# Kernel optimization log

Hardware: AMD Instinct MI355X
Metric: run time of the kernel (lower is better)

## Reference

```python
import jax, jax.numpy as jnp
import numpy as np

B, S, H, E = 4, 4096, 4096, 64
EPS = 1e-6


def setup_inputs() -> dict:
    key = jax.random.key(0)
    k1, k2 = jax.random.split(key)
    hidden_states = jax.random.normal(k1, (B, S, H), dtype=jnp.float32)
    gate_w = jax.random.normal(k2, (E, H), dtype=jnp.float32) * 0.02
    return {"hidden_states": hidden_states, "gate_w": gate_w, "C": 512}


def reference(hidden_states, gate_w, C):
    b, s, h = hidden_states.shape
    e = gate_w.shape[0]
    flat = hidden_states.reshape(-1, h)                    # [BS, H]
    logits = jnp.einsum('th,eh->te', flat, gate_w)          # [BS, E]
    # deterministic=True -> no noise added
    probs = jax.nn.softmax(logits, axis=-1)                 # [BS, E]
    # expert-choice: each expert picks top-C tokens
    _, topC_idx = jax.lax.top_k(logits.T, C)                # [E, C] token indices
    routing_map = jnp.zeros_like(logits).at[
        topC_idx, jnp.arange(e)[:, None]].set(1.0)          # [BS, E]
    # normalize_weights=True
    probs = probs * routing_map
    probs = probs / (probs.sum(axis=-1, keepdims=True) + EPS)
    # aux losses (torch .std() is unbiased -> ddof=1)
    importance = probs.sum(axis=0)                          # [E]
    imp_loss = (jnp.std(importance, ddof=1) / (importance.mean() + EPS)) ** 2
    load = routing_map.sum(axis=0)                          # [E]
    load_loss = (jnp.std(load, ddof=1) / (load.mean() + EPS)) ** 2
    aux_loss = imp_loss + load_loss
    return (probs.reshape(b, s, e), routing_map.reshape(b, s, e), aux_loss)
```

## Files before the change

### kernel.cpp

```cpp
#include <hip/hip_runtime.h>
#include <hip/hip_bf16.h>

#define BS 16384
#define HDIM 4096
#define NE 64
#define KC 64
#define TT 64
#define CAP 512
#define DELTA 2e-3f

typedef __bf16 bf16x8 __attribute__((ext_vector_type(8)));
typedef float f32x4 __attribute__((ext_vector_type(4)));
union Frag { uint4 q; bf16x8 v; };

__device__ inline unsigned f2key(float f) {
    unsigned u = __float_as_uint(f);
    return (u & 0x80000000u) ? ~u : (u | 0x80000000u);
}
__device__ inline float key2f(unsigned k) {
    unsigned u = (k & 0x80000000u) ? (k ^ 0x80000000u) : ~k;
    return __uint_as_float(u);
}
__device__ inline unsigned pack_hi(float a, float b) {
    return (__float_as_uint(a) >> 16) | (__float_as_uint(b) & 0xFFFF0000u);
}
__device__ inline float bf16_resid(float a) {
    return a - __uint_as_float(__float_as_uint(a) & 0xFFFF0000u);
}

__global__ __launch_bounds__(256) void k0_init(const float* __restrict__ W,
                                               unsigned short* __restrict__ Wh,
                                               unsigned short* __restrict__ Wl,
                                               unsigned* __restrict__ win_g,
                                               double* __restrict__ imp_g) {
    const int gtid = blockIdx.x * 256 + threadIdx.x;
    const size_t f = (size_t)gtid * 4;
    float4 w = *(const float4*)(W + f);
    uint2 hh, ll;
    hh.x = pack_hi(w.x, w.y); hh.y = pack_hi(w.z, w.w);
    ll.x = pack_hi(bf16_resid(w.x), bf16_resid(w.y));
    ll.y = pack_hi(bf16_resid(w.z), bf16_resid(w.w));
    *(uint2*)(Wh + f) = hh;
    *(uint2*)(Wl + f) = ll;
    if (gtid < NE * CAP) win_g[gtid] = 0u;
    if (gtid < NE) imp_g[gtid] = 0.0;
}

__global__ __launch_bounds__(512, 1) void k1_gemm(const float* __restrict__ A,
                                                  const unsigned short* __restrict__ Wh,
                                                  const unsigned short* __restrict__ Wl,
                                                  float* __restrict__ Lg,
                                                  unsigned* __restrict__ KeyT) {
    __shared__ __align__(16) unsigned short sbuf[2 * 18432];

    const int tid = threadIdx.x;
    const int T0 = blockIdx.x * TT;

    const int arow = tid >> 3, aseg = tid & 7;
    const int wr = (tid >> 3) & 63, wblk = tid & 7;

    const int lane = tid & 63, w = tid >> 6;
    const int m = lane & 15, q = lane >> 4;
    const int wm = w & 3;
    const int wn = w >> 2;

    const float* Aprow = A + (size_t)(T0 + arow) * HDIM + aseg * 8;
    const unsigned short* Whrow = Wh + (size_t)wr * HDIM + wblk * 8;
    const unsigned short* Wlrow = Wl + (size_t)wr * HDIM + wblk * 8;

    f32x4 acc[2] = {{0.f, 0.f, 0.f, 0.f}, {0.f, 0.f, 0.f, 0.f}};

    float4 pa0 = *(const float4*)(Aprow);
    float4 pa1 = *(const float4*)(Aprow + 4);
    uint4 pw0 = *(const uint4*)(Whrow);
    uint4 pw1 = *(const uint4*)(Wlrow);

    {
        unsigned short* B = sbuf;
        uint4 H, L;
        H.x = pack_hi(pa0.x, pa0.y); H.y = pack_hi(pa0.z, pa0.w);
        H.z = pack_hi(pa1.x, pa1.y); H.w = pack_hi(pa1.z, pa1.w);
        L.x = pack_hi(bf16_resid(pa0.x), bf16_resid(pa0.y));
        L.y = pack_hi(bf16_resid(pa0.z), bf16_resid(pa0.w));
        L.z = pack_hi(bf16_resid(pa1.x), bf16_resid(pa1.y));
        L.w = pack_hi(bf16_resid(pa1.z), bf16_resid(pa1.w));
        *(uint4*)(B + arow * 72 + aseg * 8) = H;
        *(uint4*)(B + 4608 + arow * 72 + aseg * 8) = L;
        *(uint4*)(B + 9216 + wr * 72 + wblk * 8) = pw0;
        *(uint4*)(B + 13824 + wr * 72 + wblk * 8) = pw1;
    }

    for (int c = 0; c < HDIM / KC; ++c) {
        if (c + 1 < HDIM / KC) {
            const int c0 = (c + 1) * KC;
            pa0 = *(const float4*)(Aprow + c0);
            pa1 = *(const float4*)(Aprow + c0 + 4);
            pw0 = *(const uint4*)(Whrow + c0);
            pw1 = *(const uint4*)(Wlrow + c0);
        }
        __syncthreads();
        {
            const unsigned short* B = sbuf + (c & 1) * 18432;
            const unsigned short* Ash = B + (wm * 16 + m) * 72;
            const unsigned short* Asl = Ash + 4608;
#pragma unroll
            for (int kh = 0; kh < 2; ++kh) {
                const int ko = kh * 32 + q * 8;
                Frag ah, al;
                ah.q = *(const uint4*)(Ash + ko);
                al.q = *(const uint4*)(Asl + ko);
#pragma unroll
                for (int nt = 0; nt < 2; ++nt) {
                    const int er = wn * 32 + nt * 16 + m;
                    Frag bh, bl;
                    bh.q = *(const uint4*)(B + 9216 + er * 72 + ko);
                    bl.q = *(const uint4*)(B + 13824 + er * 72 + ko);
                    acc[nt] = __builtin_amdgcn_mfma_f32_16x16x32_bf16(ah.v, bh.v, acc[nt], 0, 0, 0);
                    acc[nt] = __builtin_amdgcn_mfma_f32_16x16x32_bf16(al.v, bh.v, acc[nt], 0, 0, 0);
                    acc[nt] = __builtin_amdgcn_mfma_f32_16x16x32_bf16(ah.v, bl.v, acc[nt], 0, 0, 0);
                }
            }
        }
        if (c + 1 < HDIM / KC) {
            unsigned short* B = sbuf + ((c + 1) & 1) * 18432;
            uint4 H, L;
            H.x = pack_hi(pa0.x, pa0.y); H.y = pack_hi(pa0.z, pa0.w);
            H.z = pack_hi(pa1.x, pa1.y); H.w = pack_hi(pa1.z, pa1.w);
            L.x = pack_hi(bf16_resid(pa0.x), bf16_resid(pa0.y));
            L.y = pack_hi(bf16_resid(pa0.z), bf16_resid(pa0.w));
            L.z = pack_hi(bf16_resid(pa1.x), bf16_resid(pa1.y));
            L.w = pack_hi(bf16_resid(pa1.z), bf16_resid(pa1.w));
            *(uint4*)(B + arow * 72 + aseg * 8) = H;
            *(uint4*)(B + 4608 + arow * 72 + aseg * 8) = L;
            *(uint4*)(B + 9216 + wr * 72 + wblk * 8) = pw0;
            *(uint4*)(B + 13824 + wr * 72 + wblk * 8) = pw1;
        }
    }

    __syncthreads();
    float* Sc = (float*)sbuf;
#pragma unroll
    for (int nt = 0; nt < 2; ++nt) {
        const int e = wn * 32 + nt * 16 + m;
#pragma unroll
        for (int r = 0; r < 4; ++r) {
            const int tl = wm * 16 + q * 4 + r;
            const float v = acc[nt][r];
            Sc[tl * 68 + e] = v;
            Lg[(size_t)(T0 + tl) * NE + e] = v;
        }
    }
    __syncthreads();
    {
        const int e = tid >> 3, jj = tid & 7;
        unsigned kk[8];
#pragma unroll
        for (int r = 0; r < 8; ++r) kk[r] = f2key(Sc[(jj * 8 + r) * 68 + e]);
        uint4 v0 = {kk[0], kk[1], kk[2], kk[3]}, v1 = {kk[4], kk[5], kk[6], kk[7]};
        unsigned* dst = KeyT + (size_t)e * BS + T0 + jj * 8;
        *(uint4*)dst = v0;
        *(uint4*)(dst + 4) = v1;
    }
}

__global__ __launch_bounds__(1024) void k2_select(const unsigned* __restrict__ KeyT,
                                                  const int* __restrict__ Cptr,
                                                  unsigned* __restrict__ khi_g,
                                                  int* __restrict__ needed_g,
                                                  int* __restrict__ ncand_g,
                                                  int* __restrict__ cand_g) {
    const int e = blockIdx.x, tid = threadIdx.x;
    const int wid = tid >> 6, lane = tid & 63;
    const int C = *Cptr;
    const unsigned* col = KeyT + (size_t)e * BS;

    unsigned key[16];
#pragma unroll
    for (int j = 0; j < 16; ++j) key[j] = col[j * 1024 + tid];

    __shared__ int sred[16];
    __shared__ int s_tot;
    __shared__ int s_nc;

    unsigned K = 0;
    for (int b = 31; b >= 0; --b) {
        const unsigned T = K | (1u << b);
        int c = 0;
#pragma unroll
        for (int j = 0; j < 16; ++j) c += (key[j] >= T);
#pragma unroll
        for (int off = 32; off; off >>= 1) c += __shfl_xor(c, off);
        if (lane == 0) sred[wid] = c;
        __syncthreads();
        if (wid == 0) {
            int v = (lane < 16) ? sred[lane] : 0;
            v += __shfl_xor(v, 1); v += __shfl_xor(v, 2);
            v += __shfl_xor(v, 4); v += __shfl_xor(v, 8);
            if (lane == 0) s_tot = v;
        }
        __syncthreads();
        if (s_tot >= C) K = T;
        __syncthreads();
    }

    const float vT = key2f(K);
    const unsigned khi = f2key(vT + DELTA);
    const unsigned klo = f2key(vT - DELTA);

    int nd = 0;
#pragma unroll
    for (int j = 0; j < 16; ++j) nd += (key[j] > khi);
#pragma unroll
    for (int off = 32; off; off >>= 1) nd += __shfl_xor(nd, off);
    if (lane == 0) sred[wid] = nd;
    if (tid == 0) s_nc = 0;
    __syncthreads();
    if (wid == 0) {
        int v = (lane < 16) ? sred[lane] : 0;
        v += __shfl_xor(v, 1); v += __shfl_xor(v, 2);
        v += __shfl_xor(v, 4); v += __shfl_xor(v, 8);
        if (lane == 0) s_tot = v;
    }
    __syncthreads();
#pragma unroll
    for (int j = 0; j < 16; ++j) {
        if (key[j] >= klo && key[j] <= khi) {
            const int pos = atomicAdd(&s_nc, 1);
            if (pos < CAP) cand_g[(size_t)e * CAP + pos] = j * 1024 + tid;
        }
    }
    __syncthreads();
    if (tid == 0) {
        khi_g[e] = khi;
        needed_g[e] = C - s_tot;
        ncand_g[e] = (s_nc < CAP) ? s_nc : CAP;
    }
}

__global__ __launch_bounds__(256) void k2b_resolve(const float* __restrict__ A,
                                                   const float* __restrict__ W,
                                                   const int* __restrict__ needed_g,
                                                   const int* __restrict__ ncand_g,
                                                   const int* __restrict__ cand_g,
                                                   unsigned* __restrict__ win_g) {
    const int e = blockIdx.x, tid = threadIdx.x, w = tid >> 6, lane = tid & 63;
    int n = ncand_g[e]; if (n > CAP) n = CAP;
    int need = needed_g[e]; if (need > n) need = n; if (need < 0) need = 0;
    __shared__ double sval[CAP];
    __shared__ int sidx[CAP];
    const float* Wr = W + (size_t)e * HDIM;
    for (int c = w; c < n; c += 4) {
        const int t = cand_g[(size_t)e * CAP + c];
        const float* Ar = A + (size_t)t * HDIM;
        double ps = 0.0;
#pragma unroll 8
        for (int j = 0; j < HDIM / 64; ++j)
            ps += (double)Ar[j * 64 + lane] * (double)Wr[j * 64 + lane];
#pragma unroll
        for (int off = 32; off; off >>= 1) ps += __shfl_xor(ps, off);
        if (lane == 0) { sval[c] = ps; sidx[c] = t; }
    }
    __syncthreads();
    if (tid == 0) {
        for (int s = 0; s < need; ++s) {
            int best = -1;
            for (int c = 0; c < n; ++c) {
                if (sidx[c] < 0) continue;
                if (best < 0 || sval[c] > sval[best] ||
                    (sval[c] == sval[best] && sidx[c] < sidx[best]))
                    best = c;
            }
            const int t = sidx[best];
            win_g[(size_t)e * CAP + (t >> 5)] |= (1u << (t & 31));
            sidx[best] = -1;
        }
    }
}

__global__ __launch_bounds__(256) void k3_softmax(const float* __restrict__ Lg,
                                                  const unsigned* __restrict__ khi_g,
                                                  const unsigned* __restrict__ win_g,
                                                  float* __restrict__ probs,
                                                  float* __restrict__ out_map,
                                                  double* __restrict__ imp_g) {
    const int tid = threadIdx.x, w = tid >> 6, e = tid & 63, b = blockIdx.x;
    __shared__ unsigned skhi[64];
    __shared__ double sim[4][64];
    if (tid < 64) skhi[tid] = khi_g[tid];
    __syncthreads();
    const unsigned kh = skhi[e];
    double accim = 0.0;
#pragma unroll
    for (int it = 0; it < 4; ++it) {
        const int t = b * 16 + w * 4 + it;
        const float x = Lg[(size_t)t * NE + e];
        const unsigned key = f2key(x);
        float mfl;
        if (key > kh) mfl = 1.f;
        else mfl = (float)((win_g[(size_t)e * CAP + (t >> 5)] >> (t & 31)) & 1u);
        const float ev = expf(x);
        const float evm = ev * mfl;
        float s1 = ev, s2 = evm;
#pragma unroll
        for (int off = 32; off; off >>= 1) {
            s1 += __shfl_xor(s1, off);
            s2 += __shfl_xor(s2, off);
        }
        const float o = evm / (s2 + 1e-6f * s1);
        probs[(size_t)t * NE + e] = o;
        out_map[(size_t)t * NE + e] = mfl;
        accim += (double)o;
    }
    sim[w][e] = accim;
    __syncthreads();
    if (w == 0) atomicAdd(&imp_g[e], sim[0][e] + sim[1][e] + sim[2][e] + sim[3][e]);
}

__global__ __launch_bounds__(64) void k4_aux(const double* __restrict__ imp_g,
                                             float* __restrict__ out_aux) {
    const int e = threadIdx.x;
    const double v = imp_g[e];
    double s = v;
#pragma unroll
    for (int off = 32; off; off >>= 1) s += __shfl_xor(s, off);
    const double mean = s / 64.0;
    const double d = v - mean;
    double ss = d * d;
#pragma unroll
    for (int off = 32; off; off >>= 1) ss += __shfl_xor(ss, off);
    if (e == 0) {
        const double var = ss / 63.0;
        const double dn = mean + 1e-6;
        out_aux[0] = (float)(var / (dn * dn));
    }
}

extern "C" void kernel_launch(void* const* d_in, const int* in_sizes, int n_in,
                              void* d_out, int out_size, void* d_ws, size_t ws_size,
                              hipStream_t stream) {
    const float* A = (const float*)d_in[0];
    const float* W = (const float*)d_in[1];
    const int* Cptr = (const int*)d_in[2];

    float* out_probs = (float*)d_out;
    float* out_map = out_probs + (size_t)BS * NE;
    float* out_aux = out_map + (size_t)BS * NE;

    char* wsb = (char*)d_ws;
    float*          Lg     = (float*)wsb;
    unsigned*       KeyT   = (unsigned*)(wsb + (4ull << 20));
    unsigned short* Wh     = (unsigned short*)(wsb + (8ull << 20));
    unsigned short* Wl     = (unsigned short*)(wsb + (8ull << 20) + (512ull << 10));
    int*            cand   = (int*)(wsb + (9ull << 20));
    unsigned*       win    = (unsigned*)(wsb + (9ull << 20) + (128ull << 10));
    unsigned*       khi_g  = (unsigned*)(wsb + (9ull << 20) + (256ull << 10));
    int*            needed = (int*)(wsb + (9ull << 20) + (257ull << 10));
    int*            ncand  = (int*)(wsb + (9ull << 20) + (258ull << 10));
    double*         imp_g  = (double*)(wsb + (9ull << 20) + (259ull << 10));

    k0_init<<<256, 256, 0, stream>>>(W, Wh, Wl, win, imp_g);
    k1_gemm<<<BS / TT, 512, 0, stream>>>(A, Wh, Wl, Lg, KeyT);
    k2_select<<<NE, 1024, 0, stream>>>(KeyT, Cptr, khi_g, needed, ncand, cand);
    k2b_resolve<<<NE, 256, 0, stream>>>(A, W, needed, ncand, cand, win);
    k3_softmax<<<BS / 16, 256, 0, stream>>>(Lg, khi_g, win, out_probs, out_map, imp_g);
    k4_aux<<<1, 64, 0, stream>>>(imp_g, out_aux);
}
```

Baseline: 473.9 us.

## Shrink GEMM token tile, use per-token win bitmask, drop importance atomics

```diff
diff --git a/kernel.cpp b/kernel.cpp
--- a/kernel.cpp
+++ b/kernel.cpp
@@ -5,7 +5,7 @@
 #define HDIM 4096
 #define NE 64
 #define KC 64
-#define TT 64
+#define TT 32
 #define CAP 512
 #define DELTA 2e-3f
 
@@ -31,8 +31,7 @@
 __global__ __launch_bounds__(256) void k0_init(const float* __restrict__ W,
                                                unsigned short* __restrict__ Wh,
                                                unsigned short* __restrict__ Wl,
-                                               unsigned* __restrict__ win_g,
-                                               double* __restrict__ imp_g) {
+                                               unsigned long long* __restrict__ win_t) {
     const int gtid = blockIdx.x * 256 + threadIdx.x;
     const size_t f = (size_t)gtid * 4;
     float4 w = *(const float4*)(W + f);
@@ -42,38 +41,40 @@
     ll.y = pack_hi(bf16_resid(w.z), bf16_resid(w.w));
     *(uint2*)(Wh + f) = hh;
     *(uint2*)(Wl + f) = ll;
-    if (gtid < NE * CAP) win_g[gtid] = 0u;
-    if (gtid < NE) imp_g[gtid] = 0.0;
-}
-
-__global__ __launch_bounds__(512, 1) void k1_gemm(const float* __restrict__ A,
+    if (gtid < BS) win_t[gtid] = 0ull;
+}
+
+__global__ __launch_bounds__(256, 2) void k1_gemm(const float* __restrict__ A,
                                                   const unsigned short* __restrict__ Wh,
                                                   const unsigned short* __restrict__ Wl,
                                                   float* __restrict__ Lg,
                                                   unsigned* __restrict__ KeyT) {
-    __shared__ __align__(16) unsigned short sbuf[2 * 18432];
+    __shared__ __align__(16) unsigned short sbuf[2 * 13824];
 
     const int tid = threadIdx.x;
     const int T0 = blockIdx.x * TT;
 
     const int arow = tid >> 3, aseg = tid & 7;
-    const int wr = (tid >> 3) & 63, wblk = tid & 7;
 
     const int lane = tid & 63, w = tid >> 6;
     const int m = lane & 15, q = lane >> 4;
-    const int wm = w & 3;
-    const int wn = w >> 2;
+    const int wm = w & 1;
+    const int wn = w >> 1;
 
     const float* Aprow = A + (size_t)(T0 + arow) * HDIM + aseg * 8;
-    const unsigned short* Whrow = Wh + (size_t)wr * HDIM + wblk * 8;
-    const unsigned short* Wlrow = Wl + (size_t)wr * HDIM + wblk * 8;
 
     f32x4 acc[2] = {{0.f, 0.f, 0.f, 0.f}, {0.f, 0.f, 0.f, 0.f}};
 
     float4 pa0 = *(const float4*)(Aprow);
     float4 pa1 = *(const float4*)(Aprow + 4);
-    uint4 pw0 = *(const uint4*)(Whrow);
-    uint4 pw1 = *(const uint4*)(Wlrow);
+    uint4 pwh[2], pwl[2];
+#pragma unroll
+    for (int i = 0; i < 2; ++i) {
+        const int u = i * 256 + tid;
+        const int r = u >> 3, blk = u & 7;
+        pwh[i] = *(const uint4*)(Wh + (size_t)r * HDIM + blk * 8);
+        pwl[i] = *(const uint4*)(Wl + (size_t)r * HDIM + blk * 8);
+    }
 
     {
         unsigned short* B = sbuf;
@@ -85,9 +86,14 @@
         L.z = pack_hi(bf16_resid(pa1.x), bf16_resid(pa1.y));
         L.w = pack_hi(bf16_resid(pa1.z), bf16_resid(pa1.w));
         *(uint4*)(B + arow * 72 + aseg * 8) = H;
-        *(uint4*)(B + 4608 + arow * 72 + aseg * 8) = L;
-        *(uint4*)(B + 9216 + wr * 72 + wblk * 8) = pw0;
-        *(uint4*)(B + 13824 + wr * 72 + wblk * 8) = pw1;
+        *(uint4*)(B + 2304 + arow * 72 + aseg * 8) = L;
+#pragma unroll
+        for (int i = 0; i < 2; ++i) {
+            const int u = i * 256 + tid;
+            const int r = u >> 3, blk = u & 7;
+            *(uint4*)(B + 4608 + r * 72 + blk * 8) = pwh[i];
+            *(uint4*)(B + 9216 + r * 72 + blk * 8) = pwl[i];
+        }
     }
 
     for (int c = 0; c < HDIM / KC; ++c) {
@@ -95,14 +101,19 @@
             const int c0 = (c + 1) * KC;
             pa0 = *(const float4*)(Aprow + c0);
             pa1 = *(const float4*)(Aprow + c0 + 4);
-            pw0 = *(const uint4*)(Whrow + c0);
-            pw1 = *(const uint4*)(Wlrow + c0);
+#pragma unroll
+            for (int i = 0; i < 2; ++i) {
+                const int u = i * 256 + tid;
+                const int r = u >> 3, blk = u & 7;
+                pwh[i] = *(const uint4*)(Wh + (size_t)r * HDIM + c0 + blk * 8);
+                pwl[i] = *(const uint4*)(Wl + (size_t)r * HDIM + c0 + blk * 8);
+            }
         }
         __syncthreads();
         {
-            const unsigned short* B = sbuf + (c & 1) * 18432;
+            const unsigned short* B = sbuf + (c & 1) * 13824;
             const unsigned short* Ash = B + (wm * 16 + m) * 72;
-            const unsigned short* Asl = Ash + 4608;
+            const unsigned short* Asl = Ash + 2304;
 #pragma unroll
             for (int kh = 0; kh < 2; ++kh) {
                 const int ko = kh * 32 + q * 8;
@@ -113,8 +124,8 @@
                 for (int nt = 0; nt < 2; ++nt) {
                     const int er = wn * 32 + nt * 16 + m;
                     Frag bh, bl;
-                    bh.q = *(const uint4*)(B + 9216 + er * 72 + ko);
-                    bl.q = *(const uint4*)(B + 13824 + er * 72 + ko);
+                    bh.q = *(const uint4*)(B + 4608 + er * 72 + ko);
+                    bl.q = *(const uint4*)(B + 9216 + er * 72 + ko);
                     acc[nt] = __builtin_amdgcn_mfma_f32_16x16x32_bf16(ah.v, bh.v, acc[nt], 0, 0, 0);
                     acc[nt] = __builtin_amdgcn_mfma_f32_16x16x32_bf16(al.v, bh.v, acc[nt], 0, 0, 0);
                     acc[nt] = __builtin_amdgcn_mfma_f32_16x16x32_bf16(ah.v, bl.v, acc[nt], 0, 0, 0);
@@ -122,7 +133,7 @@
             }
         }
         if (c + 1 < HDIM / KC) {
-            unsigned short* B = sbuf + ((c + 1) & 1) * 18432;
+            unsigned short* B = sbuf + ((c + 1) & 1) * 13824;
             uint4 H, L;
             H.x = pack_hi(pa0.x, pa0.y); H.y = pack_hi(pa0.z, pa0.w);
             H.z = pack_hi(pa1.x, pa1.y); H.w = pack_hi(pa1.z, pa1.w);
@@ -131,9 +142,14 @@
             L.z = pack_hi(bf16_resid(pa1.x), bf16_resid(pa1.y));
             L.w = pack_hi(bf16_resid(pa1.z), bf16_resid(pa1.w));
             *(uint4*)(B + arow * 72 + aseg * 8) = H;
-            *(uint4*)(B + 4608 + arow * 72 + aseg * 8) = L;
-            *(uint4*)(B + 9216 + wr * 72 + wblk * 8) = pw0;
-            *(uint4*)(B + 13824 + wr * 72 + wblk * 8) = pw1;
+            *(uint4*)(B + 2304 + arow * 72 + aseg * 8) = L;
+#pragma unroll
+            for (int i = 0; i < 2; ++i) {
+                const int u = i * 256 + tid;
+                const int r = u >> 3, blk = u & 7;
+                *(uint4*)(B + 4608 + r * 72 + blk * 8) = pwh[i];
+                *(uint4*)(B + 9216 + r * 72 + blk * 8) = pwl[i];
+            }
         }
     }
 
@@ -152,7 +168,7 @@
     }
     __syncthreads();
     {
-        const int e = tid >> 3, jj = tid & 7;
+        const int e = tid >> 2, jj = tid & 3;
         unsigned kk[8];
 #pragma unroll
         for (int r = 0; r < 8; ++r) kk[r] = f2key(Sc[(jj * 8 + r) * 68 + e]);
@@ -242,7 +258,7 @@
                                                    const int* __restrict__ needed_g,
                                                    const int* __restrict__ ncand_g,
                                                    const int* __restrict__ cand_g,
-                                                   unsigned* __restrict__ win_g) {
+                                                   unsigned long long* __restrict__ win_t) {
     const int e = blockIdx.x, tid = threadIdx.x, w = tid >> 6, lane = tid & 63;
     int n = ncand_g[e]; if (n > CAP) n = CAP;
     int need = needed_g[e]; if (need > n) need = n; if (need < 0) need = 0;
@@ -271,7 +287,7 @@
                     best = c;
             }
             const int t = sidx[best];
-            win_g[(size_t)e * CAP + (t >> 5)] |= (1u << (t & 31));
+            atomicOr(&win_t[t], 1ull << e);
             sidx[best] = -1;
         }
     }
@@ -279,10 +295,10 @@
 
 __global__ __launch_bounds__(256) void k3_softmax(const float* __restrict__ Lg,
                                                   const unsigned* __restrict__ khi_g,
-                                                  const unsigned* __restrict__ win_g,
+                                                  const unsigned long long* __restrict__ win_t,
                                                   float* __restrict__ probs,
                                                   float* __restrict__ out_map,
-                                                  double* __restrict__ imp_g) {
+                                                  double* __restrict__ imp_partial) {
     const int tid = threadIdx.x, w = tid >> 6, e = tid & 63, b = blockIdx.x;
     __shared__ unsigned skhi[64];
     __shared__ double sim[4][64];
@@ -291,13 +307,13 @@
     const unsigned kh = skhi[e];
     double accim = 0.0;
 #pragma unroll
-    for (int it = 0; it < 4; ++it) {
-        const int t = b * 16 + w * 4 + it;
+    for (int it = 0; it < 16; ++it) {
+        const int t = b * 64 + it * 4 + w;
         const float x = Lg[(size_t)t * NE + e];
         const unsigned key = f2key(x);
         float mfl;
         if (key > kh) mfl = 1.f;
-        else mfl = (float)((win_g[(size_t)e * CAP + (t >> 5)] >> (t & 31)) & 1u);
+        else mfl = (float)((win_t[t] >> e) & 1ull);
         const float ev = expf(x);
         const float evm = ev * mfl;
         float s1 = ev, s2 = evm;
@@ -313,13 +329,15 @@
     }
     sim[w][e] = accim;
     __syncthreads();
-    if (w == 0) atomicAdd(&imp_g[e], sim[0][e] + sim[1][e] + sim[2][e] + sim[3][e]);
-}
-
-__global__ __launch_bounds__(64) void k4_aux(const double* __restrict__ imp_g,
+    if (w == 0)
+        imp_partial[(size_t)b * NE + e] = sim[0][e] + sim[1][e] + sim[2][e] + sim[3][e];
+}
+
+__global__ __launch_bounds__(64) void k4_aux(const double* __restrict__ imp_partial,
                                              float* __restrict__ out_aux) {
     const int e = threadIdx.x;
-    const double v = imp_g[e];
+    double v = 0.0;
+    for (int b = 0; b < 256; ++b) v += imp_partial[(size_t)b * NE + e];
     double s = v;
 #pragma unroll
     for (int off = 32; off; off >>= 1) s += __shfl_xor(s, off);
@@ -347,21 +365,21 @@
     float* out_aux = out_map + (size_t)BS * NE;
 
     char* wsb = (char*)d_ws;
-    float*          Lg     = (float*)wsb;
-    unsigned*       KeyT   = (unsigned*)(wsb + (4ull << 20));
-    unsigned short* Wh     = (unsigned short*)(wsb + (8ull << 20));
-    unsigned short* Wl     = (unsigned short*)(wsb + (8ull << 20) + (512ull << 10));
-    int*            cand   = (int*)(wsb + (9ull << 20));
-    unsigned*       win    = (unsigned*)(wsb + (9ull << 20) + (128ull << 10));
-    unsigned*       khi_g  = (unsigned*)(wsb + (9ull << 20) + (256ull << 10));
-    int*            needed = (int*)(wsb + (9ull << 20) + (257ull << 10));
-    int*            ncand  = (int*)(wsb + (9ull << 20) + (258ull << 10));
-    double*         imp_g  = (double*)(wsb + (9ull << 20) + (259ull << 10));
-
-    k0_init<<<256, 256, 0, stream>>>(W, Wh, Wl, win, imp_g);
-    k1_gemm<<<BS / TT, 512, 0, stream>>>(A, Wh, Wl, Lg, KeyT);
+    float*              Lg     = (float*)wsb;
+    unsigned*           KeyT   = (unsigned*)(wsb + (4ull << 20));
+    unsigned short*     Wh     = (unsigned short*)(wsb + (8ull << 20));
+    unsigned short*     Wl     = (unsigned short*)(wsb + (8ull << 20) + (512ull << 10));
+    int*                cand   = (int*)(wsb + (9ull << 20));
+    unsigned long long* win_t  = (unsigned long long*)(wsb + (9ull << 20) + (128ull << 10));
+    unsigned*           khi_g  = (unsigned*)(wsb + (9ull << 20) + (256ull << 10));
+    int*                needed = (int*)(wsb + (9ull << 20) + (257ull << 10));
+    int*                ncand  = (int*)(wsb + (9ull << 20) + (258ull << 10));
+    double*             imp_p  = (double*)(wsb + (9ull << 20) + (512ull << 10));
+
+    k0_init<<<256, 256, 0, stream>>>(W, Wh, Wl, win_t);
+    k1_gemm<<<BS / TT, 256, 0, stream>>>(A, Wh, Wl, Lg, KeyT);
     k2_select<<<NE, 1024, 0, stream>>>(KeyT, Cptr, khi_g, needed, ncand, cand);
-    k2b_resolve<<<NE, 256, 0, stream>>>(A, W, needed, ncand, cand, win);
-    k3_softmax<<<BS / 16, 256, 0, stream>>>(Lg, khi_g, win, out_probs, out_map, imp_g);
-    k4_aux<<<1, 64, 0, stream>>>(imp_g, out_aux);
-}
+    k2b_resolve<<<NE, 256, 0, stream>>>(A, W, needed, ncand, cand, win_t);
+    k3_softmax<<<BS / 64, 256, 0, stream>>>(Lg, khi_g, win_t, out_probs, out_map, imp_p);
+    k4_aux<<<1, 64, 0, stream>>>(imp_p, out_aux);
+}
```

New measurement: 464.0 us. 1.02x faster.
